# Kernel tuning notes

Hardware: AMD Instinct MI355X
Metric: run time of the kernel (lower is better)

Reference implementation:

```python
import jax, jax.numpy as jnp
import numpy as np

B = 8          # sequences in prefill batch
S = 1024       # tokens per sequence (uniform ragged batch)
T = B * S      # total prefill tokens
HID = 2560
H = 32         # query heads
KV = 32        # kv heads (MHA for default Phi config)
D = 80         # head_dim = hidden // heads
ROT = 40       # rotary dim = 0.5 * head_dim
D_PAD = 128    # flashinfer padded head dim
SCALE = 1.0 / np.sqrt(D_PAD)  # flashinfer default sm_scale uses padded head dim


def setup_inputs() -> dict:
    key = jax.random.key(0)
    ks = jax.random.split(key, 7)
    hidden_states = jax.random.normal(ks[0], (T, HID), dtype=jnp.float32)
    # rotary tables: one row per token position (random stand-ins, same math)
    cos = jax.random.uniform(ks[1], (T, ROT // 2), dtype=jnp.float32)
    sin = jax.random.uniform(ks[2], (T, ROT // 2), dtype=jnp.float32)
    w_qkv = jax.random.normal(ks[3], ((H + 2 * KV) * D, HID), dtype=jnp.float32) * 0.02
    b_qkv = jax.random.normal(ks[4], ((H + 2 * KV) * D,), dtype=jnp.float32) * 0.02
    w_dense = jax.random.normal(ks[5], (HID, HID), dtype=jnp.float32) * 0.02
    b_dense = jax.random.normal(ks[6], (HID,), dtype=jnp.float32) * 0.02
    return {"hidden_states": hidden_states, "cos": cos, "sin": sin,
            "w_qkv": w_qkv, "b_qkv": b_qkv, "w_dense": w_dense, "b_dense": b_dense}


def _apply_partial_rope(x, cos, sin):
    # x: [T, heads, D]; NeoX rotate-half on the first ROT dims only
    half = ROT // 2
    x1 = x[:, :, :half]
    x2 = x[:, :, half:ROT]
    xp = x[:, :, ROT:]
    c = cos[:, None, :]
    s = sin[:, None, :]
    return jnp.concatenate([x1 * c - x2 * s, x2 * c + x1 * s, xp], axis=-1)


def reference(hidden_states, cos, sin, w_qkv, b_qkv, w_dense, b_dense):
    # fused QKV projection
    qkv = hidden_states @ w_qkv.T + b_qkv              # [T, (H+2KV)*D]
    q, k, v = jnp.split(qkv, [H * D, H * D + KV * D], axis=1)
    q = q.reshape(T, H, D)
    k = k.reshape(T, KV, D)
    v = v.reshape(T, KV, D)
    # inline partial RoPE
    q = _apply_partial_rope(q, cos, sin)
    k = _apply_partial_rope(k, cos, sin)
    # paged prefill attention == per-sequence causal attention over appended KV
    qb = q.reshape(B, S, H, D)
    kb = k.reshape(B, S, KV, D)
    vb = v.reshape(B, S, KV, D)
    scores = jnp.einsum('bqhd,bkhd->bhqk', qb, kb) * SCALE   # [B,H,S,S]
    causal = jnp.tril(jnp.ones((S, S), dtype=bool))
    scores = jnp.where(causal[None, None], scores, jnp.finfo(scores.dtype).min)
    probs = jax.nn.softmax(scores, axis=-1)
    attn = jnp.einsum('bhqk,bkhd->bqhd', probs, vb)          # [B,S,H,D]
    attn = attn.reshape(T, HID)
    return attn @ w_dense.T + b_dense
```

## Files before the change

kernel.cpp:

```cpp
#include <hip/hip_runtime.h>
#include <hip/hip_bf16.h>
#include <cmath>
#include <stdint.h>

#define B_SZ 8
#define S_LEN 1024
#define T_LEN (B_SZ * S_LEN)
#define HID 2560
#define NH 32
#define DH 80
#define ROT 40
#define RHALF 20
#define DP 96
#define NQKV 7680
#define SCALE 0.08838834764831844f

typedef unsigned short u16;
typedef short bf16x8 __attribute__((ext_vector_type(8)));
typedef float f32x4 __attribute__((ext_vector_type(4)));

#define AS1C(p) ((const __attribute__((address_space(1))) void*)(p))
#define AS3(p)  ((__attribute__((address_space(3))) void*)(p))

__device__ inline u16 f2b(float f) {
  __hip_bfloat16 h = __float2bfloat16(f);
  return __builtin_bit_cast(unsigned short, h);
}
__device__ inline float b2f(u16 u) {
  return __bfloat162float(__builtin_bit_cast(__hip_bfloat16, u));
}

__global__ void cast_bf16_kernel(const float* __restrict__ x, u16* __restrict__ y, int n4) {
  int stride = gridDim.x * blockDim.x;
  for (int i = blockIdx.x * blockDim.x + threadIdx.x; i < n4; i += stride) {
    float4 v = ((const float4*)x)[i];
    u16 a = f2b(v.x), b = f2b(v.y), c = f2b(v.z), d = f2b(v.w);
    uint2 o;
    o.x = (unsigned)a | ((unsigned)b << 16);
    o.y = (unsigned)c | ((unsigned)d << 16);
    ((uint2*)y)[i] = o;
  }
}

template<int OUT_BF16>
__global__ __launch_bounds__(256) void gemm_bt_kernel(
    const u16* __restrict__ A, const u16* __restrict__ Bm,
    const float* __restrict__ bias, void* __restrict__ Cv,
    int M, int N, int K)
{
  __shared__ __align__(16) u16 As[128 * 64];
  __shared__ __align__(16) u16 Bs[128 * 64];
  int tid = threadIdx.x, w = tid >> 6, lane = tid & 63;
  int mb = blockIdx.y << 7, nb = blockIdx.x << 7;
  int wr = (w >> 1) << 6, wc = (w & 1) << 6;
  int col = lane & 15, quad = lane >> 4;

  f32x4 acc[4][4];
  const f32x4 fz = {0.f, 0.f, 0.f, 0.f};
  for (int i = 0; i < 4; i++)
    for (int j = 0; j < 4; j++) acc[i][j] = fz;

  int c0 = __builtin_amdgcn_readfirstlane(4 * w);
  int rr = lane >> 3;
  int swu = (lane & 7) ^ rr;
  int kof = swu * 8;
  const u16* aP = A + (size_t)(mb + 8 * c0 + rr) * K + kof;
  const u16* bP = Bm + (size_t)(nb + 8 * c0 + rr) * K + kof;
  int rxor = col & 7;

  for (int kb = 0; kb < K; kb += 64) {
#pragma unroll
    for (int i = 0; i < 4; i++) {
      __builtin_amdgcn_global_load_lds(AS1C(aP + (size_t)8 * i * K + kb),
                                       AS3(&As[(c0 + i) * 512]), 16, 0, 0);
      __builtin_amdgcn_global_load_lds(AS1C(bP + (size_t)8 * i * K + kb),
                                       AS3(&Bs[(c0 + i) * 512]), 16, 0, 0);
    }
    __syncthreads();
#pragma unroll
    for (int kh = 0; kh < 2; kh++) {
      int uoff = ((quad + 4 * kh) ^ rxor) * 8;
      bf16x8 af[4], bfv[4];
#pragma unroll
      for (int i = 0; i < 4; i++)
        af[i] = *(const bf16x8*)&As[(wr + i * 16 + col) * 64 + uoff];
#pragma unroll
      for (int i = 0; i < 4; i++)
        bfv[i] = *(const bf16x8*)&Bs[(wc + i * 16 + col) * 64 + uoff];
#pragma unroll
      for (int mi = 0; mi < 4; mi++)
#pragma unroll
        for (int ni = 0; ni < 4; ni++)
          acc[mi][ni] = __builtin_amdgcn_mfma_f32_16x16x32_bf16(af[mi], bfv[ni], acc[mi][ni], 0, 0, 0);
    }
    __syncthreads();
  }

  for (int ni = 0; ni < 4; ni++) {
    int n = nb + wc + ni * 16 + col;
    float bv = bias[n];
    for (int mi = 0; mi < 4; mi++) {
      int mrow = mb + wr + mi * 16 + quad * 4;
      for (int r = 0; r < 4; r++) {
        float v = acc[mi][ni][r] + bv;
        if (OUT_BF16)
          ((u16*)Cv)[(size_t)(mrow + r) * N + n] = f2b(v);
        else
          ((float*)Cv)[(size_t)(mrow + r) * N + n] = v;
      }
    }
  }
}

__global__ void rope_qk_kernel(const u16* __restrict__ qkv,
                               const float* __restrict__ cosd,
                               const float* __restrict__ sind,
                               u16* __restrict__ Q96, u16* __restrict__ K96) {
  int t = blockIdx.x;
  int b = t >> 10, s = t & 1023;
  __shared__ float cs[RHALF], sn[RHALF];
  int tid = threadIdx.x;
  if (tid < RHALF) cs[tid] = cosd[t * RHALF + tid];
  else if (tid < 2 * RHALF) sn[tid - RHALF] = sind[t * RHALF + (tid - RHALF)];
  __syncthreads();
  for (int i = tid; i < 2 * NH * DP; i += 256) {
    int sel = (i >= NH * DP) ? 1 : 0;
    int ii = i - sel * NH * DP;
    int hh = ii / DP, d = ii - hh * DP;
    const u16* src = qkv + (size_t)t * NQKV + sel * HID + hh * DH;
    float v;
    if (d < RHALF)      v = b2f(src[d]) * cs[d] - b2f(src[d + RHALF]) * sn[d];
    else if (d < ROT)   v = b2f(src[d]) * cs[d - RHALF] + b2f(src[d - RHALF]) * sn[d - RHALF];
    else if (d < DH)    v = b2f(src[d]);
    else                v = 0.f;
    if (!sel) v *= SCALE;
    u16* dst = sel ? K96 : Q96;
    dst[((size_t)(b * NH + hh) * S_LEN + s) * DP + d] = f2b(v);
  }
}

__global__ void v_trans_kernel(const u16* __restrict__ qkv, u16* __restrict__ Vt) {
  int blk = blockIdx.x;
  int st = blk & 15, bh = blk >> 4;
  int b = bh >> 5, h = bh & 31;
  int s0 = st * 64;
  __shared__ __align__(16) u16 tile[64][88];
  int tid = threadIdx.x;
  for (int c = tid; c < 640; c += 256) {
    int r = c / 10, cc = c - (c / 10) * 10;
    *(uint4*)&tile[r][cc * 8] =
        *(const uint4*)(qkv + (size_t)(b * S_LEN + s0 + r) * NQKV + 2 * HID + h * DH + cc * 8);
  }
  __syncthreads();
  for (int i = tid; i < 5120; i += 256) {
    int d = i >> 6, ss = i & 63;
    Vt[((size_t)bh * DH + d) * S_LEN + s0 + ss] = tile[ss][d];
  }
}

__global__ __launch_bounds__(256) void flash_kernel(
    const u16* __restrict__ Q, const u16* __restrict__ K,
    const u16* __restrict__ Vt, u16* __restrict__ Oo) {
  int qt = blockIdx.x, bh = blockIdx.y;
  int b = bh >> 5, h = bh & 31;
  int tid = threadIdx.x, w = tid >> 6, lane = tid & 63;
  int col = lane & 15, quad = lane >> 4;
  int qw = qt * 128 + w * 32;

  __shared__ __align__(16) u16 Ks[64][104];
  __shared__ __align__(16) u16 Vs[96][72];
  __shared__ __align__(16) u16 Ps[4][32][72];

  for (int i = tid; i < 16 * 64; i += 256) {
    int r = 80 + (i >> 6), k = i & 63;
    Vs[r][k] = (r == 80) ? (u16)0x3F80 : (u16)0;
  }

  bf16x8 qf[2][3];
#pragma unroll
  for (int m = 0; m < 2; m++) {
    const u16* qrow = Q + ((size_t)bh * S_LEN + qw + m * 16 + col) * DP;
#pragma unroll
    for (int kk = 0; kk < 3; kk++)
      qf[m][kk] = *(const bf16x8*)(qrow + kk * 32 + quad * 8);
  }
  const f32x4 fz = {0.f, 0.f, 0.f, 0.f};
  f32x4 o[2][6];
#pragma unroll
  for (int m = 0; m < 2; m++)
#pragma unroll
    for (int n = 0; n < 6; n++) o[m][n] = fz;

  const u16* kbase0 = K + (size_t)bh * S_LEN * DP;
  const u16* vbase0 = Vt + (size_t)bh * DH * S_LEN;
  int nt = 2 * qt + 2;
  for (int kt = 0; kt < nt; kt++) {
    const u16* kbase = kbase0 + kt * 64 * DP;
    for (int c = tid; c < 768; c += 256) {
      int r = c / 12, cc = c - (c / 12) * 12;
      *(uint4*)&Ks[r][cc * 8] = *(const uint4*)(kbase + r * DP + cc * 8);
    }
    const u16* vbase = vbase0 + kt * 64;
    for (int c = tid; c < 640; c += 256) {
      int d = c >> 3, cc = c & 7;
      *(uint4*)&Vs[d][cc * 8] = *(const uint4*)(vbase + (size_t)d * S_LEN + cc * 8);
    }
    __syncthreads();
    int k0 = kt * 64;
    if (k0 <= qw + 31) {
#pragma unroll
      for (int m = 0; m < 2; m++) {
        int rowbase = qw + m * 16;
        f32x4 s[4];
#pragma unroll
        for (int n = 0; n < 4; n++) {
          f32x4 acc = fz;
#pragma unroll
          for (int kk = 0; kk < 3; kk++) {
            bf16x8 kf = *(const bf16x8*)&Ks[n * 16 + col][kk * 32 + quad * 8];
            acc = __builtin_amdgcn_mfma_f32_16x16x32_bf16(qf[m][kk], kf, acc, 0, 0, 0);
          }
          s[n] = acc;
        }
        if (k0 + 63 > rowbase) {
#pragma unroll
          for (int n = 0; n < 4; n++) {
            int key = k0 + n * 16 + col;
#pragma unroll
            for (int r = 0; r < 4; r++)
              if (key > rowbase + quad * 4 + r) s[n][r] = -INFINITY;
          }
        }
#pragma unroll
        for (int n = 0; n < 4; n++)
#pragma unroll
          for (int r = 0; r < 4; r++) {
            float p = __expf(fminf(s[n][r], 30.f));
            Ps[w][m * 16 + quad * 4 + r][n * 16 + col] = f2b(p);
          }
      }
      asm volatile("s_waitcnt lgkmcnt(0)" ::: "memory");
#pragma unroll
      for (int m = 0; m < 2; m++)
#pragma unroll
        for (int kk = 0; kk < 2; kk++) {
          bf16x8 pf = *(const bf16x8*)&Ps[w][m * 16 + col][kk * 32 + quad * 8];
#pragma unroll
          for (int n2 = 0; n2 < 6; n2++) {
            bf16x8 vf = *(const bf16x8*)&Vs[n2 * 16 + col][kk * 32 + quad * 8];
            o[m][n2] = __builtin_amdgcn_mfma_f32_16x16x32_bf16(pf, vf, o[m][n2], 0, 0, 0);
          }
        }
    }
    __syncthreads();
  }
  int src = lane & 48;
#pragma unroll
  for (int m = 0; m < 2; m++)
#pragma unroll
    for (int r = 0; r < 4; r++) {
      float l = __shfl(o[m][5][r], src);
      float inv = 1.f / l;
      int t = b * S_LEN + qw + m * 16 + quad * 4 + r;
#pragma unroll
      for (int n2 = 0; n2 < 5; n2++)
        Oo[(size_t)t * HID + h * DH + n2 * 16 + col] = f2b(o[m][n2][r] * inv);
    }
}

extern "C" void kernel_launch(void* const* d_in, const int* in_sizes, int n_in,
                              void* d_out, int out_size, void* d_ws, size_t ws_size,
                              hipStream_t stream) {
  const float* hidden  = (const float*)d_in[0];
  const float* cosd    = (const float*)d_in[1];
  const float* sind    = (const float*)d_in[2];
  const float* w_qkv   = (const float*)d_in[3];
  const float* b_qkv   = (const float*)d_in[4];
  const float* w_dense = (const float*)d_in[5];
  const float* b_dense = (const float*)d_in[6];
  float* out = (float*)d_out;

  char* ws = (char*)d_ws;
  u16* hid_bf    = (u16*)(ws);
  u16* wqkv_bf   = (u16*)(ws + 41943040ull);
  u16* Q96       = (u16*)(ws);
  u16* qkv_bf    = (u16*)(ws + 81264640ull);
  u16* attn_bf   = (u16*)(ws + 81264640ull);
  u16* wdense_bf = (u16*)(ws + 81264640ull + 41943040ull);
  u16* K96       = (u16*)(ws + 81264640ull + 125829120ull);
  u16* Vt        = (u16*)(ws + 81264640ull + 125829120ull + 50331648ull);

  cast_bf16_kernel<<<2048, 256, 0, stream>>>(hidden, hid_bf, T_LEN * HID / 4);
  cast_bf16_kernel<<<2048, 256, 0, stream>>>(w_qkv, wqkv_bf, NQKV * HID / 4);
  gemm_bt_kernel<1><<<dim3(NQKV / 128, T_LEN / 128), 256, 0, stream>>>(
      hid_bf, wqkv_bf, b_qkv, qkv_bf, T_LEN, NQKV, HID);
  rope_qk_kernel<<<T_LEN, 256, 0, stream>>>(qkv_bf, cosd, sind, Q96, K96);
  v_trans_kernel<<<4096, 256, 0, stream>>>(qkv_bf, Vt);
  flash_kernel<<<dim3(8, 256), 256, 0, stream>>>(Q96, K96, Vt, attn_bf);
  cast_bf16_kernel<<<512, 256, 0, stream>>>(w_dense, wdense_bf, HID * HID / 4);
  gemm_bt_kernel<0><<<dim3(HID / 128, T_LEN / 128), 256, 0, stream>>>(
      attn_bf, wdense_bf, b_dense, out, T_LEN, HID, HID);
}
```

Measured before the change: 1.167 ms.

## Replace 128x128 GEMM with double-buffered 256x256 tile, 512-thread pipelined kernel

Both projection GEMMs now use a 256x256 output tile per block with 8 waves, each computing a 128x64 sub-tile. The kernel double-buffers A and B half-tiles in 128KB of LDS and issues async global-to-LDS loads for the next k-steps in between four MFMA phases. It uses explicit vmcnt/lgkmcnt waits, barriers and s_setprio around the MFMA bursts. The aim is to hide global load latency and raise arithmetic intensity. The cost is heavier LDS and register use, and fewer blocks for the dense GEMM (10x32 tiles).

```diff
diff --git a/kernel.cpp b/kernel.cpp
--- a/kernel.cpp
+++ b/kernel.cpp
@@ -43,64 +43,158 @@
 }
 
 template<int OUT_BF16>
-__global__ __launch_bounds__(256) void gemm_bt_kernel(
+__global__ __launch_bounds__(512, 2) void gemm256_kernel(
     const u16* __restrict__ A, const u16* __restrict__ Bm,
     const float* __restrict__ bias, void* __restrict__ Cv,
     int M, int N, int K)
 {
-  __shared__ __align__(16) u16 As[128 * 64];
-  __shared__ __align__(16) u16 Bs[128 * 64];
+  __shared__ __align__(16) u16 smem[65536];
+  u16* As = smem;
+  u16* Bs = smem + 32768;
+  const int NT = K >> 6;
+
   int tid = threadIdx.x, w = tid >> 6, lane = tid & 63;
-  int mb = blockIdx.y << 7, nb = blockIdx.x << 7;
-  int wr = (w >> 1) << 6, wc = (w & 1) << 6;
+  int wm = w >> 2;
+  int wn = w & 3;
   int col = lane & 15, quad = lane >> 4;
-
-  f32x4 acc[4][4];
-  const f32x4 fz = {0.f, 0.f, 0.f, 0.f};
-  for (int i = 0; i < 4; i++)
-    for (int j = 0; j < 4; j++) acc[i][j] = fz;
-
-  int c0 = __builtin_amdgcn_readfirstlane(4 * w);
+  int mb = blockIdx.y << 8, nb = blockIdx.x << 8;
+
   int rr = lane >> 3;
   int swu = (lane & 7) ^ rr;
-  int kof = swu * 8;
-  const u16* aP = A + (size_t)(mb + 8 * c0 + rr) * K + kof;
-  const u16* bP = Bm + (size_t)(nb + 8 * c0 + rr) * K + kof;
+  int c0 = __builtin_amdgcn_readfirstlane(2 * w);
+  const u16* aP = A + (size_t)(mb + 16 * w + rr) * K + 8 * swu;
+  const u16* bP = Bm + (size_t)(nb + 16 * w + rr) * K + 8 * swu;
+
   int rxor = col & 7;
-
-  for (int kb = 0; kb < K; kb += 64) {
-#pragma unroll
-    for (int i = 0; i < 4; i++) {
-      __builtin_amdgcn_global_load_lds(AS1C(aP + (size_t)8 * i * K + kb),
-                                       AS3(&As[(c0 + i) * 512]), 16, 0, 0);
-      __builtin_amdgcn_global_load_lds(AS1C(bP + (size_t)8 * i * K + kb),
-                                       AS3(&Bs[(c0 + i) * 512]), 16, 0, 0);
-    }
-    __syncthreads();
-#pragma unroll
-    for (int kh = 0; kh < 2; kh++) {
-      int uoff = ((quad + 4 * kh) ^ rxor) * 8;
-      bf16x8 af[4], bfv[4];
-#pragma unroll
-      for (int i = 0; i < 4; i++)
-        af[i] = *(const bf16x8*)&As[(wr + i * 16 + col) * 64 + uoff];
-#pragma unroll
-      for (int i = 0; i < 4; i++)
-        bfv[i] = *(const bf16x8*)&Bs[(wc + i * 16 + col) * 64 + uoff];
-#pragma unroll
-      for (int mi = 0; mi < 4; mi++)
-#pragma unroll
-        for (int ni = 0; ni < 4; ni++)
-          acc[mi][ni] = __builtin_amdgcn_mfma_f32_16x16x32_bf16(af[mi], bfv[ni], acc[mi][ni], 0, 0, 0);
-    }
-    __syncthreads();
-  }
-
+  int u0 = (quad ^ rxor) * 8;
+  int u1 = ((quad + 4) ^ rxor) * 8;
+  const u16* aBase0 = As + wm * 8192 + col * 64;
+  const u16* bBase0 = Bs + (wn >> 1) * 8192 + ((wn & 1) * 64 + col) * 64;
+
+  f32x4 acc[8][4];
+  const f32x4 fz = {0.f, 0.f, 0.f, 0.f};
+#pragma unroll
+  for (int i = 0; i < 8; i++)
+#pragma unroll
+    for (int j = 0; j < 4; j++) acc[i][j] = fz;
+
+#define STAGE_A(kt, h) do { \
+    const u16* _s = aP + (size_t)(h) * 128 * K + (size_t)(kt) * 64; \
+    u16* _d = As + (((kt) & 1) * 2 + (h)) * 8192 + c0 * 512; \
+    __builtin_amdgcn_global_load_lds(AS1C(_s), AS3(_d), 16, 0, 0); \
+    __builtin_amdgcn_global_load_lds(AS1C(_s + 8 * (size_t)K), AS3(_d + 512), 16, 0, 0); \
+  } while (0)
+#define STAGE_B(kt, h) do { \
+    const u16* _s = bP + (size_t)(h) * 128 * K + (size_t)(kt) * 64; \
+    u16* _d = Bs + (((kt) & 1) * 2 + (h)) * 8192 + c0 * 512; \
+    __builtin_amdgcn_global_load_lds(AS1C(_s), AS3(_d), 16, 0, 0); \
+    __builtin_amdgcn_global_load_lds(AS1C(_s + 8 * (size_t)K), AS3(_d + 512), 16, 0, 0); \
+  } while (0)
+
+  STAGE_A(0, 0); STAGE_A(0, 1); STAGE_B(0, 0); STAGE_B(0, 1);
+  STAGE_B(1, 0); STAGE_A(1, 0);
+  asm volatile("s_waitcnt vmcnt(4)" ::: "memory");
+  __builtin_amdgcn_s_barrier();
+
+  bf16x8 af[4][2];
+  bf16x8 bfv[4][2];
+
+  for (int kt = 0; kt < NT; kt++) {
+    const int buf = kt & 1;
+    const u16* aB = aBase0 + buf * 16384;
+    const u16* bB = bBase0 + buf * 16384;
+
+#pragma unroll
+    for (int mi = 0; mi < 4; mi++) {
+      af[mi][0] = *(const bf16x8*)(aB + mi * 1024 + u0);
+      af[mi][1] = *(const bf16x8*)(aB + mi * 1024 + u1);
+    }
+#pragma unroll
+    for (int ni = 0; ni < 2; ni++) {
+      bfv[ni][0] = *(const bf16x8*)(bB + ni * 1024 + u0);
+      bfv[ni][1] = *(const bf16x8*)(bB + ni * 1024 + u1);
+    }
+    if (kt + 1 < NT) STAGE_A(kt + 1, 1);
+    __builtin_amdgcn_s_barrier();
+    asm volatile("s_waitcnt lgkmcnt(0)" ::: "memory");
+    __builtin_amdgcn_s_setprio(1);
+#pragma unroll
+    for (int mi = 0; mi < 4; mi++)
+#pragma unroll
+      for (int ni = 0; ni < 2; ni++)
+#pragma unroll
+        for (int kh = 0; kh < 2; kh++)
+          acc[mi][ni] = __builtin_amdgcn_mfma_f32_16x16x32_bf16(af[mi][kh], bfv[ni][kh], acc[mi][ni], 0, 0, 0);
+    __builtin_amdgcn_s_setprio(0);
+    __builtin_amdgcn_s_barrier();
+
+#pragma unroll
+    for (int ni = 2; ni < 4; ni++) {
+      bfv[ni][0] = *(const bf16x8*)(bB + ni * 1024 + u0);
+      bfv[ni][1] = *(const bf16x8*)(bB + ni * 1024 + u1);
+    }
+    if (kt + 1 < NT) STAGE_B(kt + 1, 1);
+    __builtin_amdgcn_s_barrier();
+    asm volatile("s_waitcnt lgkmcnt(0)" ::: "memory");
+    __builtin_amdgcn_s_setprio(1);
+#pragma unroll
+    for (int mi = 0; mi < 4; mi++)
+#pragma unroll
+      for (int ni = 2; ni < 4; ni++)
+#pragma unroll
+        for (int kh = 0; kh < 2; kh++)
+          acc[mi][ni] = __builtin_amdgcn_mfma_f32_16x16x32_bf16(af[mi][kh], bfv[ni][kh], acc[mi][ni], 0, 0, 0);
+    __builtin_amdgcn_s_setprio(0);
+    __builtin_amdgcn_s_barrier();
+
+#pragma unroll
+    for (int mi = 0; mi < 4; mi++) {
+      af[mi][0] = *(const bf16x8*)(aB + (mi + 4) * 1024 + u0);
+      af[mi][1] = *(const bf16x8*)(aB + (mi + 4) * 1024 + u1);
+    }
+    if (kt + 2 < NT) STAGE_B(kt + 2, 0);
+    __builtin_amdgcn_s_barrier();
+    asm volatile("s_waitcnt lgkmcnt(0)" ::: "memory");
+    __builtin_amdgcn_s_setprio(1);
+#pragma unroll
+    for (int mi = 0; mi < 4; mi++)
+#pragma unroll
+      for (int ni = 0; ni < 2; ni++)
+#pragma unroll
+        for (int kh = 0; kh < 2; kh++)
+          acc[4 + mi][ni] = __builtin_amdgcn_mfma_f32_16x16x32_bf16(af[mi][kh], bfv[ni][kh], acc[4 + mi][ni], 0, 0, 0);
+    __builtin_amdgcn_s_setprio(0);
+    __builtin_amdgcn_s_barrier();
+
+    if (kt + 2 < NT) {
+      STAGE_A(kt + 2, 0);
+      asm volatile("s_waitcnt vmcnt(4)" ::: "memory");
+    } else {
+      asm volatile("s_waitcnt vmcnt(0)" ::: "memory");
+    }
+    __builtin_amdgcn_s_barrier();
+    __builtin_amdgcn_s_setprio(1);
+#pragma unroll
+    for (int mi = 0; mi < 4; mi++)
+#pragma unroll
+      for (int ni = 2; ni < 4; ni++)
+#pragma unroll
+        for (int kh = 0; kh < 2; kh++)
+          acc[4 + mi][ni] = __builtin_amdgcn_mfma_f32_16x16x32_bf16(af[mi][kh], bfv[ni][kh], acc[4 + mi][ni], 0, 0, 0);
+    __builtin_amdgcn_s_setprio(0);
+    __builtin_amdgcn_s_barrier();
+  }
+#undef STAGE_A
+#undef STAGE_B
+
+#pragma unroll
   for (int ni = 0; ni < 4; ni++) {
-    int n = nb + wc + ni * 16 + col;
+    int n = nb + wn * 64 + ni * 16 + col;
     float bv = bias[n];
-    for (int mi = 0; mi < 4; mi++) {
-      int mrow = mb + wr + mi * 16 + quad * 4;
+#pragma unroll
+    for (int mi = 0; mi < 8; mi++) {
+      int mrow = mb + wm * 128 + mi * 16 + quad * 4;
+#pragma unroll
       for (int r = 0; r < 4; r++) {
         float v = acc[mi][ni][r] + bv;
         if (OUT_BF16)
@@ -292,12 +386,12 @@
 
   cast_bf16_kernel<<<2048, 256, 0, stream>>>(hidden, hid_bf, T_LEN * HID / 4);
   cast_bf16_kernel<<<2048, 256, 0, stream>>>(w_qkv, wqkv_bf, NQKV * HID / 4);
-  gemm_bt_kernel<1><<<dim3(NQKV / 128, T_LEN / 128), 256, 0, stream>>>(
+  gemm256_kernel<1><<<dim3(NQKV / 256, T_LEN / 256), 512, 0, stream>>>(
       hid_bf, wqkv_bf, b_qkv, qkv_bf, T_LEN, NQKV, HID);
   rope_qk_kernel<<<T_LEN, 256, 0, stream>>>(qkv_bf, cosd, sind, Q96, K96);
   v_trans_kernel<<<4096, 256, 0, stream>>>(qkv_bf, Vt);
   flash_kernel<<<dim3(8, 256), 256, 0, stream>>>(Q96, K96, Vt, attn_bf);
   cast_bf16_kernel<<<512, 256, 0, stream>>>(w_dense, wdense_bf, HID * HID / 4);
-  gemm_bt_kernel<0><<<dim3(HID / 128, T_LEN / 128), 256, 0, stream>>>(
+  gemm256_kernel<0><<<dim3(HID / 256, T_LEN / 256), 512, 0, stream>>>(
       attn_bf, wdense_bf, b_dense, out, T_LEN, HID, HID);
 }
```

Result: faster. 1.026 ms, median of 2 (-12.1%).
